# Optimization experiments

Measured on AMD Instinct MI355X. Metric: run time of the kernel, lower is better.

Reference implementation:

```python
import math
import jax
import jax.numpy as jnp
import numpy as np

DECAY_RATE = 0.99
LOG_CLAMP_MIN = -10.0


def setup_inputs() -> dict:
    key = jax.random.key(0)
    k0, k1, k2, k3, k4, k5 = jax.random.split(key, 6)
    B, S, D, N = 32, 4096, 256, 64
    return {
        "query": jax.random.normal(k0, (B, S, D), dtype=jnp.float32),
        "memory": jax.random.normal(k1, (1, N, D), dtype=jnp.float32),
        "importance": jax.random.uniform(k2, (1, N), dtype=jnp.float32),
        "age": jax.random.uniform(k3, (1, N), dtype=jnp.float32) * 10.0,
        # torch.nn.Linear weights are [out_features, in_features]; applied as x @ W.T
        "W_q": jax.random.normal(k4, (D, D), dtype=jnp.float32) / jnp.sqrt(D).astype(jnp.float32),
        "W_k": jax.random.normal(k5, (D, D), dtype=jnp.float32) / jnp.sqrt(D).astype(jnp.float32),
        "top_k": 8,
    }


def reference(query, memory, importance, age, W_q, W_k, top_k):
    # MemoryBank.read(): top-k masked attention over a small memory bank
    # query: [B, S, D]; memory: [1, N, D]; importance/age: [1, N]
    D = query.shape[-1]
    N = memory.shape[1]
    mem = memory[0]          # [N, D] (buffer is batch-broadcast in torch via expand)

    q = query @ W_q.T                      # [B, S, D]
    k = mem @ W_k.T                        # [N, D]
    scores = jnp.einsum("bsd,nd->bsn", q, k) / jnp.sqrt(jnp.asarray(D, query.dtype))

    # importance-decay bias, log-clamped at -10
    eff_imp = importance[0] * (DECAY_RATE ** age[0])           # [N]
    scores = scores + jnp.maximum(jnp.log(eff_imp), LOG_CLAMP_MIN)[None, None, :]

    if top_k < N:
        _, topk_idx = jax.lax.top_k(scores, top_k)             # [B, S, k]
        # scatter 1.0 at top-k indices (N is small, one-hot sum is cheap)
        mask = jax.nn.one_hot(topk_idx, N, dtype=scores.dtype).sum(axis=-2)  # [B, S, N]
        scores = jnp.where(mask > 0, scores, -jnp.inf)

    attn_weights = jax.nn.softmax(scores, axis=-1)             # [B, S, N]
    retrieved = jnp.einsum("bsn,nd->bsd", attn_weights, mem)   # [B, S, D]
    return retrieved, attn_weights
```

## Files before the change

### kernel.cpp

```cpp
#include <hip/hip_runtime.h>
#include <hip/hip_bf16.h>

#define DD 256
#define NM 64

typedef unsigned long long u64;
typedef float v2f __attribute__((ext_vector_type(2)));

struct v2x2 { v2f lo, hi; };
static __device__ __forceinline__ v2x2 splitf4(float4 f) {
    union { float4 a; v2x2 b; } u; u.a = f; return u.b;
}

#define PK_FMA_SPLATLO(acc, q2, c2) \
    asm("v_pk_fma_f32 %0, %1, %2, %0 op_sel:[0,0,0] op_sel_hi:[0,1,1]" \
        : "+v"(acc) : "v"(q2), "v"(c2))
#define PK_FMA_SPLATHI(acc, q2, c2) \
    asm("v_pk_fma_f32 %0, %1, %2, %0 op_sel:[1,0,0] op_sel_hi:[1,1,1]" \
        : "+v"(acc) : "v"(q2), "v"(c2))

__global__ __launch_bounds__(256) void prep_tr(
    const float* __restrict__ Wq, const float* __restrict__ Wk,
    float* __restrict__ wqt, float* __restrict__ wkt)
{
    const int o = blockIdx.x;
    const int d = threadIdx.x;
    if (blockIdx.y == 0) wqt[d * DD + o] = Wq[o * DD + d];
    else                 wkt[d * DD + o] = Wk[o * DD + d];
}

__global__ __launch_bounds__(256) void prep_kT(
    const float* __restrict__ mem, const float* __restrict__ wkt,
    const float* __restrict__ imp, const float* __restrict__ age,
    float* __restrict__ kT4, float* __restrict__ bias)
{
    const int n = blockIdx.x;
    const int o = threadIdx.x;
    const float* mrow = mem + n * DD;
    float acc = 0.f;
    for (int d = 0; d < DD; ++d)
        acc = fmaf(mrow[d], wkt[d * DD + o], acc);
    kT4[(o >> 2) * (NM * 4) + n * 4 + (o & 3)] = acc;

    if (o == 0) {
        double eff = (double)imp[n] * pow(0.99, (double)age[n]);
        float b = (float)log(eff);
        if (!(b >= -10.0f)) b = -10.0f;
        bias[n] = b;
    }
}

__global__ __launch_bounds__(256, 2) void qgemm4(
    const float* __restrict__ query,
    const float4* __restrict__ wqt4,
    float* __restrict__ qout,
    int M)
{
    __shared__ float q_lds[32 * DD];
    __shared__ float wq_lds[2][8 * 256];

    const int t = threadIdx.x;
    const int l = t & 63;
    const int w = __builtin_amdgcn_readfirstlane((int)(t >> 6));
    const int row0 = blockIdx.x * 32;

    {
        const float4* q4g = reinterpret_cast<const float4*>(query);
#pragma unroll
        for (int i = 0; i < 8; ++i) {
            const int idx = i * 256 + t;
            const int r = idx >> 6, c4 = idx & 63;
            int gr = row0 + r; if (gr > M - 1) gr = M - 1;
            *reinterpret_cast<float4*>(&q_lds[r * DD + c4 * 4]) =
                q4g[(size_t)gr * 64 + c4];
        }
    }
    {
        const float4 s0 = wqt4[t];
        const float4 s1 = wqt4[256 + t];
        reinterpret_cast<float4*>(wq_lds[0])[t]       = s0;
        reinterpret_cast<float4*>(wq_lds[0])[256 + t] = s1;
    }
    __syncthreads();

    v2f a01[8], a23[8];
#pragma unroll
    for (int rr = 0; rr < 8; ++rr) { a01[rr] = (v2f)(0.f); a23[rr] = (v2f)(0.f); }

    const float* qbase = &q_lds[(w * 8) * DD];

    for (int c = 0; c < 32; ++c) {
        const int cn = (c + 1) & 31;
        const float4 n0 = wqt4[cn * 512 + t];
        const float4 n1 = wqt4[cn * 512 + 256 + t];

        {
            const float4* wb = reinterpret_cast<const float4*>(wq_lds[c & 1]);
            float4 cw[8];
#pragma unroll
            for (int i = 0; i < 8; ++i) cw[i] = wb[i * 64 + l];
            const v2x2 c0 = splitf4(cw[0]), c1 = splitf4(cw[1]);
            const v2x2 c2 = splitf4(cw[2]), c3 = splitf4(cw[3]);
            const v2x2 c4 = splitf4(cw[4]), c5 = splitf4(cw[5]);
            const v2x2 c6 = splitf4(cw[6]), c7 = splitf4(cw[7]);
#pragma unroll
            for (int rr = 0; rr < 8; ++rr) {
                const float4 qqA = *reinterpret_cast<const float4*>(
                    qbase + rr * DD + c * 8);
                const float4 qqB = *reinterpret_cast<const float4*>(
                    qbase + rr * DD + c * 8 + 4);
                const v2x2 qA = splitf4(qqA);
                const v2x2 qB = splitf4(qqB);
                PK_FMA_SPLATLO(a01[rr], qA.lo, c0.lo);
                PK_FMA_SPLATLO(a23[rr], qA.lo, c0.hi);
                PK_FMA_SPLATHI(a01[rr], qA.lo, c1.lo);
                PK_FMA_SPLATHI(a23[rr], qA.lo, c1.hi);
                PK_FMA_SPLATLO(a01[rr], qA.hi, c2.lo);
                PK_FMA_SPLATLO(a23[rr], qA.hi, c2.hi);
                PK_FMA_SPLATHI(a01[rr], qA.hi, c3.lo);
                PK_FMA_SPLATHI(a23[rr], qA.hi, c3.hi);
                PK_FMA_SPLATLO(a01[rr], qB.lo, c4.lo);
                PK_FMA_SPLATLO(a23[rr], qB.lo, c4.hi);
                PK_FMA_SPLATHI(a01[rr], qB.lo, c5.lo);
                PK_FMA_SPLATHI(a23[rr], qB.lo, c5.hi);
                PK_FMA_SPLATLO(a01[rr], qB.hi, c6.lo);
                PK_FMA_SPLATLO(a23[rr], qB.hi, c6.hi);
                PK_FMA_SPLATHI(a01[rr], qB.hi, c7.lo);
                PK_FMA_SPLATHI(a23[rr], qB.hi, c7.hi);
            }
        }
        {
            float4* dst = reinterpret_cast<float4*>(wq_lds[(c + 1) & 1]);
            dst[t]       = n0;
            dst[256 + t] = n1;
        }
        __syncthreads();
    }

#pragma unroll
    for (int rr = 0; rr < 8; ++rr) {
        const int grow = row0 + w * 8 + rr;
        if (grow < M) {
            float4 v; v.x = a01[rr].x; v.y = a01[rr].y; v.z = a23[rr].x; v.w = a23[rr].y;
            *reinterpret_cast<float4*>(&qout[(size_t)grow * DD + 4 * l]) = v;
        }
    }
}

__global__ __launch_bounds__(512, 2) void scores_b(
    const float* __restrict__ qin,
    const float4* __restrict__ kT44,
    const float* __restrict__ bias,
    float* __restrict__ sout,
    int M)
{
    __shared__ float q_lds[64 * DD];
    const int t = threadIdx.x;
    const int l = t & 63;
    const int w = __builtin_amdgcn_readfirstlane((int)(t >> 6));
    const int row0 = blockIdx.x * 64;

    {
        const float4* q4g = reinterpret_cast<const float4*>(qin);
#pragma unroll
        for (int i = 0; i < 8; ++i) {
            const int idx = i * 512 + t;
            const int r = idx >> 6, c4 = idx & 63;
            int gr = row0 + r; if (gr > M - 1) gr = M - 1;
            *reinterpret_cast<float4*>(&q_lds[r * DD + ((c4 ^ r) & 63) * 4]) =
                q4g[(size_t)gr * 64 + c4];
        }
    }
    __syncthreads();

    const int nb = w * 8;
    float sc[8];
#pragma unroll
    for (int j = 0; j < 8; ++j) sc[j] = 0.f;

    for (int og = 0; og < DD / 4; ++og) {
        const float4 q4 = *reinterpret_cast<const float4*>(
            &q_lds[l * DD + (((og ^ l) & 63) << 2)]);
        const float4* ktp = kT44 + og * NM + nb;
#pragma unroll
        for (int j = 0; j < 8; ++j) {
            const float4 kt = ktp[j];
            float v = sc[j];
            v = fmaf(q4.x, kt.x, v);
            v = fmaf(q4.y, kt.y, v);
            v = fmaf(q4.z, kt.z, v);
            v = fmaf(q4.w, kt.w, v);
            sc[j] = v;
        }
    }
    __syncthreads();

    float* s_tmp = q_lds;
#pragma unroll
    for (int j = 0; j < 8; ++j)
        s_tmp[l * NM + ((nb + j + l) & 63)] = sc[j] * 0.0625f + bias[nb + j];
    __syncthreads();

#pragma unroll
    for (int i = 0; i < 8; ++i) {
        const int idx = i * 512 + t;
        const int r = idx >> 6, n = idx & 63;
        const int grow = row0 + r;
        if (grow < M) sout[(size_t)grow * NM + n] = s_tmp[r * NM + ((n + r) & 63)];
    }
}

#define FR 128
__global__ __launch_bounds__(256, 2) void fin3(
    const float* __restrict__ mem,
    const int* __restrict__ topk_p,
    float* __restrict__ out_ret,
    float* __restrict__ out_attn,
    int M)
{
    __shared__ float s_lds[FR * NM];
    __shared__ int   sel_i[FR * 16];
    __shared__ float sel_w[FR * 16];

    const int t = threadIdx.x;
    const int l = t & 63;
    const int w = __builtin_amdgcn_readfirstlane((int)(t >> 6));
    const int row0 = blockIdx.x * FR;
    const int k = *topk_p;

    {
#pragma unroll
        for (int i = 0; i < (FR * NM / 4) / 256; ++i) {
            const int idx = i * 256 + t;
            const int r = idx >> 4, c4 = idx & 15;
            int gr = row0 + r; if (gr > M - 1) gr = M - 1;
            const float4 v = *reinterpret_cast<const float4*>(
                &out_attn[(size_t)gr * NM + c4 * 4]);
            s_lds[r * NM + ((c4 * 4 + 0 + r) & 63)] = v.x;
            s_lds[r * NM + ((c4 * 4 + 1 + r) & 63)] = v.y;
            s_lds[r * NM + ((c4 * 4 + 2 + r) & 63)] = v.z;
            s_lds[r * NM + ((c4 * 4 + 3 + r) & 63)] = v.w;
        }
    }
    __syncthreads();

    if (t < FR) {
        const int r = t;
        float sv[NM];
#pragma unroll
        for (int n = 0; n < NM; ++n) sv[n] = s_lds[r * NM + ((n + r) & 63)];

        if (k < NM) {
            const int kk = k < 16 ? k : 16;
            u64 taken = 0ull;
            float mmax = 0.f, Z = 0.f;
            for (int i = 0; i < kk; ++i) {
                float m = -1.0e30f;
                int idx = 0;
#pragma unroll
                for (int n = 0; n < NM; ++n) {
                    const bool avail  = ((taken >> n) & 1ull) == 0ull;
                    const bool better = avail && (sv[n] > m);
                    m   = better ? sv[n] : m;
                    idx = better ? n : idx;
                }
                taken |= (1ull << idx);
                if (i == 0) mmax = m;
                const float wv = expf(m - mmax);
                Z += wv;
                sel_i[r * 16 + i] = idx;
                sel_w[r * 16 + i] = wv;
            }
#pragma unroll
            for (int n = 0; n < NM; ++n) s_lds[r * NM + ((n + r) & 63)] = 0.f;
            for (int i = 0; i < kk; ++i) {
                const float wz = sel_w[r * 16 + i] / Z;
                sel_w[r * 16 + i] = wz;
                s_lds[r * NM + ((sel_i[r * 16 + i] + r) & 63)] = wz;
            }
        } else {
            float m = -1.0e30f;
#pragma unroll
            for (int n = 0; n < NM; ++n) m = sv[n] > m ? sv[n] : m;
            float Z = 0.f;
#pragma unroll
            for (int n = 0; n < NM; ++n) Z += expf(sv[n] - m);
#pragma unroll
            for (int n = 0; n < NM; ++n) s_lds[r * NM + ((n + r) & 63)] = expf(sv[n] - m) / Z;
        }
    }
    __syncthreads();

#pragma unroll
    for (int i = 0; i < (FR * NM) / 256; ++i) {
        const int idx = i * 256 + t;
        const int r = idx >> 6, n = idx & 63;
        const int grow = row0 + r;
        if (grow < M) out_attn[(size_t)grow * NM + n] = s_lds[r * NM + ((n + r) & 63)];
    }

    {
        const float4* mem4 = reinterpret_cast<const float4*>(mem);
        const int kk = k < 16 ? k : 16;
#pragma unroll 1
        for (int rr = 0; rr < FR / 4; ++rr) {
            const int r    = w * (FR / 4) + rr;
            const int grow = row0 + r;
            if (grow >= M) continue;
            float4 acc; acc.x = 0.f; acc.y = 0.f; acc.z = 0.f; acc.w = 0.f;
            if (k < NM) {
                for (int i = 0; i < kk; ++i) {
                    const int   mi = sel_i[r * 16 + i];
                    const float wz = sel_w[r * 16 + i];
                    const float4 mv = mem4[mi * 64 + l];
                    acc.x = fmaf(wz, mv.x, acc.x);
                    acc.y = fmaf(wz, mv.y, acc.y);
                    acc.z = fmaf(wz, mv.z, acc.z);
                    acc.w = fmaf(wz, mv.w, acc.w);
                }
            } else {
                for (int n = 0; n < NM; ++n) {
                    const float wz = s_lds[r * NM + ((n + r) & 63)];
                    const float4 mv = mem4[n * 64 + l];
                    acc.x = fmaf(wz, mv.x, acc.x);
                    acc.y = fmaf(wz, mv.y, acc.y);
                    acc.z = fmaf(wz, mv.z, acc.z);
                    acc.w = fmaf(wz, mv.w, acc.w);
                }
            }
            *reinterpret_cast<float4*>(&out_ret[(size_t)grow * DD + 4 * l]) = acc;
        }
    }
}

extern "C" void kernel_launch(void* const* d_in, const int* in_sizes, int n_in,
                              void* d_out, int out_size, void* d_ws, size_t ws_size,
                              hipStream_t stream) {
    const float* query      = (const float*)d_in[0];
    const float* memory     = (const float*)d_in[1];
    const float* importance = (const float*)d_in[2];
    const float* age        = (const float*)d_in[3];
    const float* Wq         = (const float*)d_in[4];
    const float* Wk         = (const float*)d_in[5];
    const int*   topk       = (const int*)d_in[6];

    const int M = in_sizes[0] / DD;

    float* kT4  = (float*)d_ws;
    float* bias = kT4 + (size_t)DD * NM;
    float* wqt  = bias + 64;
    float* wkt  = wqt + (size_t)DD * DD;

    hipLaunchKernelGGL(prep_tr, dim3(DD, 2), dim3(DD), 0, stream,
                       Wq, Wk, wqt, wkt);
    hipLaunchKernelGGL(prep_kT, dim3(NM), dim3(DD), 0, stream,
                       memory, wkt, importance, age, kT4, bias);

    float* out_ret  = (float*)d_out;
    float* out_attn = out_ret + (size_t)M * DD;

    hipLaunchKernelGGL(qgemm4, dim3((M + 31) / 32), dim3(256), 0, stream,
                       query, (const float4*)wqt, out_ret, M);
    hipLaunchKernelGGL(scores_b, dim3((M + 63) / 64), dim3(512), 0, stream,
                       out_ret, (const float4*)kT4, bias, out_attn, M);
    hipLaunchKernelGGL(fin3, dim3((M + FR - 1) / FR), dim3(256), 0, stream,
                       memory, topk, out_ret, out_attn, M);
}
```

Measured before the change: 397.1 us.

## Fuse query projection into scores kernel, keeping projected q in LDS

The separate query-projection GEMM kernel is removed. The scores kernel now loads raw query rows into LDS, computes q = query·Wq^T in registers with packed FMAs whose weight operand comes from scalar registers (wave-uniform loads), and writes the result back into the swizzled LDS tile before the score loop. This avoids writing the projected q to global memory and reading it back, and saves one kernel launch. In exchange, each lane computes a 64-row by 32-column slice with 32 accumulators per lane and reads weights through the scalar cache, which could limit throughput.

```diff
diff --git a/kernel.cpp b/kernel.cpp
--- a/kernel.cpp
+++ b/kernel.cpp
@@ -12,12 +12,12 @@
     union { float4 a; v2x2 b; } u; u.a = f; return u.b;
 }
 
-#define PK_FMA_SPLATLO(acc, q2, c2) \
+#define PK_FMA_SPLATLO_S(acc, q2, c2) \
     asm("v_pk_fma_f32 %0, %1, %2, %0 op_sel:[0,0,0] op_sel_hi:[0,1,1]" \
-        : "+v"(acc) : "v"(q2), "v"(c2))
-#define PK_FMA_SPLATHI(acc, q2, c2) \
+        : "+v"(acc) : "v"(q2), "s"(c2))
+#define PK_FMA_SPLATHI_S(acc, q2, c2) \
     asm("v_pk_fma_f32 %0, %1, %2, %0 op_sel:[1,0,0] op_sel_hi:[1,1,1]" \
-        : "+v"(acc) : "v"(q2), "v"(c2))
+        : "+v"(acc) : "v"(q2), "s"(c2))
 
 __global__ __launch_bounds__(256) void prep_tr(
     const float* __restrict__ Wq, const float* __restrict__ Wk,
@@ -50,118 +50,23 @@
     }
 }
 
-__global__ __launch_bounds__(256, 2) void qgemm4(
+__global__ __launch_bounds__(512, 2) void qs6(
     const float* __restrict__ query,
-    const float4* __restrict__ wqt4,
-    float* __restrict__ qout,
-    int M)
-{
-    __shared__ float q_lds[32 * DD];
-    __shared__ float wq_lds[2][8 * 256];
-
-    const int t = threadIdx.x;
-    const int l = t & 63;
-    const int w = __builtin_amdgcn_readfirstlane((int)(t >> 6));
-    const int row0 = blockIdx.x * 32;
-
-    {
-        const float4* q4g = reinterpret_cast<const float4*>(query);
-#pragma unroll
-        for (int i = 0; i < 8; ++i) {
-            const int idx = i * 256 + t;
-            const int r = idx >> 6, c4 = idx & 63;
-            int gr = row0 + r; if (gr > M - 1) gr = M - 1;
-            *reinterpret_cast<float4*>(&q_lds[r * DD + c4 * 4]) =
-                q4g[(size_t)gr * 64 + c4];
-        }
-    }
-    {
-        const float4 s0 = wqt4[t];
-        const float4 s1 = wqt4[256 + t];
-        reinterpret_cast<float4*>(wq_lds[0])[t]       = s0;
-        reinterpret_cast<float4*>(wq_lds[0])[256 + t] = s1;
-    }
-    __syncthreads();
-
-    v2f a01[8], a23[8];
-#pragma unroll
-    for (int rr = 0; rr < 8; ++rr) { a01[rr] = (v2f)(0.f); a23[rr] = (v2f)(0.f); }
-
-    const float* qbase = &q_lds[(w * 8) * DD];
-
-    for (int c = 0; c < 32; ++c) {
-        const int cn = (c + 1) & 31;
-        const float4 n0 = wqt4[cn * 512 + t];
-        const float4 n1 = wqt4[cn * 512 + 256 + t];
-
-        {
-            const float4* wb = reinterpret_cast<const float4*>(wq_lds[c & 1]);
-            float4 cw[8];
-#pragma unroll
-            for (int i = 0; i < 8; ++i) cw[i] = wb[i * 64 + l];
-            const v2x2 c0 = splitf4(cw[0]), c1 = splitf4(cw[1]);
-            const v2x2 c2 = splitf4(cw[2]), c3 = splitf4(cw[3]);
-            const v2x2 c4 = splitf4(cw[4]), c5 = splitf4(cw[5]);
-            const v2x2 c6 = splitf4(cw[6]), c7 = splitf4(cw[7]);
-#pragma unroll
-            for (int rr = 0; rr < 8; ++rr) {
-                const float4 qqA = *reinterpret_cast<const float4*>(
-                    qbase + rr * DD + c * 8);
-                const float4 qqB = *reinterpret_cast<const float4*>(
-                    qbase + rr * DD + c * 8 + 4);
-                const v2x2 qA = splitf4(qqA);
-                const v2x2 qB = splitf4(qqB);
-                PK_FMA_SPLATLO(a01[rr], qA.lo, c0.lo);
-                PK_FMA_SPLATLO(a23[rr], qA.lo, c0.hi);
-                PK_FMA_SPLATHI(a01[rr], qA.lo, c1.lo);
-                PK_FMA_SPLATHI(a23[rr], qA.lo, c1.hi);
-                PK_FMA_SPLATLO(a01[rr], qA.hi, c2.lo);
-                PK_FMA_SPLATLO(a23[rr], qA.hi, c2.hi);
-                PK_FMA_SPLATHI(a01[rr], qA.hi, c3.lo);
-                PK_FMA_SPLATHI(a23[rr], qA.hi, c3.hi);
-                PK_FMA_SPLATLO(a01[rr], qB.lo, c4.lo);
-                PK_FMA_SPLATLO(a23[rr], qB.lo, c4.hi);
-                PK_FMA_SPLATHI(a01[rr], qB.lo, c5.lo);
-                PK_FMA_SPLATHI(a23[rr], qB.lo, c5.hi);
-                PK_FMA_SPLATLO(a01[rr], qB.hi, c6.lo);
-                PK_FMA_SPLATLO(a23[rr], qB.hi, c6.hi);
-                PK_FMA_SPLATHI(a01[rr], qB.hi, c7.lo);
-                PK_FMA_SPLATHI(a23[rr], qB.hi, c7.hi);
-            }
-        }
-        {
-            float4* dst = reinterpret_cast<float4*>(wq_lds[(c + 1) & 1]);
-            dst[t]       = n0;
-            dst[256 + t] = n1;
-        }
-        __syncthreads();
-    }
-
-#pragma unroll
-    for (int rr = 0; rr < 8; ++rr) {
-        const int grow = row0 + w * 8 + rr;
-        if (grow < M) {
-            float4 v; v.x = a01[rr].x; v.y = a01[rr].y; v.z = a23[rr].x; v.w = a23[rr].y;
-            *reinterpret_cast<float4*>(&qout[(size_t)grow * DD + 4 * l]) = v;
-        }
-    }
-}
-
-__global__ __launch_bounds__(512, 2) void scores_b(
-    const float* __restrict__ qin,
+    const float* __restrict__ wqt,
     const float4* __restrict__ kT44,
     const float* __restrict__ bias,
     float* __restrict__ sout,
     int M)
 {
     __shared__ float q_lds[64 * DD];
+
     const int t = threadIdx.x;
     const int l = t & 63;
     const int w = __builtin_amdgcn_readfirstlane((int)(t >> 6));
     const int row0 = blockIdx.x * 64;
 
     {
-        const float4* q4g = reinterpret_cast<const float4*>(qin);
+        const float4* q4g = reinterpret_cast<const float4*>(query);
 #pragma unroll
         for (int i = 0; i < 8; ++i) {
             const int idx = i * 512 + t;
@@ -170,6 +75,47 @@
             *reinterpret_cast<float4*>(&q_lds[r * DD + ((c4 ^ r) & 63) * 4]) =
                 q4g[(size_t)gr * 64 + c4];
         }
+    }
+    __syncthreads();
+
+    v2f p[16];
+#pragma unroll
+    for (int j = 0; j < 16; ++j) p[j] = (v2f)(0.f);
+
+    {
+        const float* qrow = &q_lds[l * DD];
+        for (int og = 0; og < DD / 4; ++og) {
+            const float4 q4 = *reinterpret_cast<const float4*>(
+                &qrow[((og ^ l) & 63) << 2]);
+            const v2x2 qh = splitf4(q4);
+            const int d0 = og * 4;
+            const v2f* w0 = reinterpret_cast<const v2f*>(
+                wqt + (size_t)(d0 + 0) * DD + 32 * w);
+            const v2f* w1 = reinterpret_cast<const v2f*>(
+                wqt + (size_t)(d0 + 1) * DD + 32 * w);
+            const v2f* w2 = reinterpret_cast<const v2f*>(
+                wqt + (size_t)(d0 + 2) * DD + 32 * w);
+            const v2f* w3 = reinterpret_cast<const v2f*>(
+                wqt + (size_t)(d0 + 3) * DD + 32 * w);
+#pragma unroll
+            for (int j = 0; j < 16; ++j) PK_FMA_SPLATLO_S(p[j], qh.lo, w0[j]);
+#pragma unroll
+            for (int j = 0; j < 16; ++j) PK_FMA_SPLATHI_S(p[j], qh.lo, w1[j]);
+#pragma unroll
+            for (int j = 0; j < 16; ++j) PK_FMA_SPLATLO_S(p[j], qh.hi, w2[j]);
+#pragma unroll
+            for (int j = 0; j < 16; ++j) PK_FMA_SPLATHI_S(p[j], qh.hi, w3[j]);
+        }
+    }
+    __syncthreads();
+
+#pragma unroll
+    for (int j4 = 0; j4 < 8; ++j4) {
+        const int c4 = w * 8 + j4;
+        float4 v;
+        v.x = p[2 * j4].x;     v.y = p[2 * j4].y;
+        v.z = p[2 * j4 + 1].x; v.w = p[2 * j4 + 1].y;
+        *reinterpret_cast<float4*>(&q_lds[l * DD + ((c4 ^ l) & 63) * 4]) = v;
     }
     __syncthreads();
 
@@ -359,10 +305,8 @@
     float* out_ret  = (float*)d_out;
     float* out_attn = out_ret + (size_t)M * DD;
 
-    hipLaunchKernelGGL(qgemm4, dim3((M + 31) / 32), dim3(256), 0, stream,
-                       query, (const float4*)wqt, out_ret, M);
-    hipLaunchKernelGGL(scores_b, dim3((M + 63) / 64), dim3(512), 0, stream,
-                       out_ret, (const float4*)kT4, bias, out_attn, M);
+    hipLaunchKernelGGL(qs6, dim3((M + 63) / 64), dim3(512), 0, stream,
+                       query, wqt, (const float4*)kT4, bias, out_attn, M);
     hipLaunchKernelGGL(fin3, dim3((M + FR - 1) / FR), dim3(256), 0, stream,
                        memory, topk, out_ret, out_attn, M);
 }
```

Measured after the change: 427.4 us. +7.6%, slower.

## Double the Q-projection row tile and stream query chunks through double-buffered LDS

Applied to the files above, without the earlier changes.

The Q-projection GEMM now gives each block 64 rows instead of 32, so each wave holds 16 rows of accumulators and every staged weight chunk is reused twice as much. The full 32x256 query tile in LDS is replaced by a small double-buffered 64x8 chunk that is prefetched alongside the weight chunk, which cuts LDS use and drops the up-front load stall. The cost is twice the accumulator registers, which could limit occupancy or cause spills at the two-blocks-per-SM bound, and the 8-byte query loads are less coalesced.

```diff
diff --git a/kernel.cpp b/kernel.cpp
--- a/kernel.cpp
+++ b/kernel.cpp
@@ -50,32 +50,28 @@
     }
 }
 
-__global__ __launch_bounds__(256, 2) void qgemm4(
+__global__ __launch_bounds__(256, 2) void qgemm5(
     const float* __restrict__ query,
     const float4* __restrict__ wqt4,
     float* __restrict__ qout,
     int M)
 {
-    __shared__ float q_lds[32 * DD];
     __shared__ float wq_lds[2][8 * 256];
+    __shared__ float qc_lds[2][64 * 8];
 
     const int t = threadIdx.x;
     const int l = t & 63;
     const int w = __builtin_amdgcn_readfirstlane((int)(t >> 6));
-    const int row0 = blockIdx.x * 32;
+    const int row0 = blockIdx.x * 64;
+
+    const int sr = t >> 2;
+    const int sd = (t & 3) * 2;
+    int srow = row0 + sr; if (srow > M - 1) srow = M - 1;
+    const float* qsrc = query + (size_t)srow * DD + sd;
 
     {
-        const float4* q4g = reinterpret_cast<const float4*>(query);
-#pragma unroll
-        for (int i = 0; i < 8; ++i) {
-            const int idx = i * 256 + t;
-            const int r = idx >> 6, c4 = idx & 63;
-            int gr = row0 + r; if (gr > M - 1) gr = M - 1;
-            *reinterpret_cast<float4*>(&q_lds[r * DD + c4 * 4]) =
-                q4g[(size_t)gr * 64 + c4];
-        }
-    }
-    {
+        const float2 qv = *reinterpret_cast<const float2*>(qsrc);
+        *reinterpret_cast<float2*>(&qc_lds[0][sr * 8 + sd]) = qv;
         const float4 s0 = wqt4[t];
         const float4 s1 = wqt4[256 + t];
         reinterpret_cast<float4*>(wq_lds[0])[t]       = s0;
@@ -83,14 +79,13 @@
     }
     __syncthreads();
 
-    v2f a01[8], a23[8];
-#pragma unroll
-    for (int rr = 0; rr < 8; ++rr) { a01[rr] = (v2f)(0.f); a23[rr] = (v2f)(0.f); }
-
-    const float* qbase = &q_lds[(w * 8) * DD];
+    v2f a01[16], a23[16];
+#pragma unroll
+    for (int rr = 0; rr < 16; ++rr) { a01[rr] = (v2f)(0.f); a23[rr] = (v2f)(0.f); }
 
     for (int c = 0; c < 32; ++c) {
         const int cn = (c + 1) & 31;
+        const float2 nq = *reinterpret_cast<const float2*>(qsrc + cn * 8);
         const float4 n0 = wqt4[cn * 512 + t];
         const float4 n1 = wqt4[cn * 512 + 256 + t];
 
@@ -103,12 +98,13 @@
             const v2x2 c2 = splitf4(cw[2]), c3 = splitf4(cw[3]);
             const v2x2 c4 = splitf4(cw[4]), c5 = splitf4(cw[5]);
             const v2x2 c6 = splitf4(cw[6]), c7 = splitf4(cw[7]);
-#pragma unroll
-            for (int rr = 0; rr < 8; ++rr) {
+            const float* qcb = &qc_lds[c & 1][(w * 16) * 8];
+#pragma unroll
+            for (int rr = 0; rr < 16; ++rr) {
                 const float4 qqA = *reinterpret_cast<const float4*>(
-                    qbase + rr * DD + c * 8);
+                    qcb + rr * 8);
                 const float4 qqB = *reinterpret_cast<const float4*>(
-                    qbase + rr * DD + c * 8 + 4);
+                    qcb + rr * 8 + 4);
                 const v2x2 qA = splitf4(qqA);
                 const v2x2 qB = splitf4(qqB);
                 PK_FMA_SPLATLO(a01[rr], qA.lo, c0.lo);
@@ -130,6 +126,7 @@
             }
         }
         {
+            *reinterpret_cast<float2*>(&qc_lds[(c + 1) & 1][sr * 8 + sd]) = nq;
             float4* dst = reinterpret_cast<float4*>(wq_lds[(c + 1) & 1]);
             dst[t]       = n0;
             dst[256 + t] = n1;
@@ -138,8 +135,8 @@
     }
 
 #pragma unroll
-    for (int rr = 0; rr < 8; ++rr) {
-        const int grow = row0 + w * 8 + rr;
+    for (int rr = 0; rr < 16; ++rr) {
+        const int grow = row0 + w * 16 + rr;
         if (grow < M) {
             float4 v; v.x = a01[rr].x; v.y = a01[rr].y; v.z = a23[rr].x; v.w = a23[rr].y;
             *reinterpret_cast<float4*>(&qout[(size_t)grow * DD + 4 * l]) = v;
@@ -359,7 +356,7 @@
     float* out_ret  = (float*)d_out;
     float* out_attn = out_ret + (size_t)M * DD;
 
-    hipLaunchKernelGGL(qgemm4, dim3((M + 31) / 32), dim3(256), 0, stream,
+    hipLaunchKernelGGL(qgemm5, dim3((M + 63) / 64), dim3(256), 0, stream,
                        query, (const float4*)wqt, out_ret, M);
     hipLaunchKernelGGL(scores_b, dim3((M + 63) / 64), dim3(512), 0, stream,
                        out_ret, (const float4*)kT4, bias, out_attn, M);
```

Measured after the change: 385.1 us. 3.0% less time.
